# Performance work log

Hardware: AMD Instinct MI355X
Metric: run time of the kernel (lower is better)

The kernel has to match this reference:

```python
import jax, jax.numpy as jnp
import numpy as np

N_NODES = 30000
N_EDGES = 480000
N_GRAPHS = 64
IN_DIM = 128
HID = 64
NEG_SLOPE = 0.2  # PyG GATConv default leaky_relu slope


def setup_inputs() -> dict:
    key = jax.random.key(0)
    ks = jax.random.split(key, 16)
    x = jax.random.normal(ks[0], (N_NODES, IN_DIM), dtype=jnp.float32)
    src = jax.random.randint(ks[1], (N_EDGES,), 0, N_NODES, dtype=jnp.int32)
    dst = jax.random.randint(ks[2], (N_EDGES,), 0, N_NODES, dtype=jnp.int32)
    edge_index = jnp.stack([src, dst], axis=0)
    # evenly-sized sorted graph assignment so every graph id is populated
    batch = (jnp.arange(N_NODES, dtype=jnp.int32) * N_GRAPHS) // N_NODES
    sc1 = 1.0 / np.sqrt(IN_DIM)
    sc2 = 1.0 / np.sqrt(4 * HID)
    sc3 = 1.0 / np.sqrt(HID)
    return dict(
        x=x, edge_index=edge_index, batch=batch,
        W1=jax.random.normal(ks[3], (IN_DIM, 4 * HID), jnp.float32) * sc1,
        att_src1=jax.random.normal(ks[4], (4, HID), jnp.float32) * sc3,
        att_dst1=jax.random.normal(ks[5], (4, HID), jnp.float32) * sc3,
        b1=jnp.zeros((4 * HID,), jnp.float32),
        W2=jax.random.normal(ks[6], (4 * HID, HID), jnp.float32) * sc2,
        att_src2=jax.random.normal(ks[7], (1, HID), jnp.float32) * sc3,
        att_dst2=jax.random.normal(ks[8], (1, HID), jnp.float32) * sc3,
        b2=jnp.zeros((HID,), jnp.float32),
        w_fc1=jax.random.normal(ks[9], (HID, HID), jnp.float32) * sc3,
        b_fc1=jnp.zeros((HID,), jnp.float32),
        w_fc2=jax.random.normal(ks[10], (HID, 2), jnp.float32) * sc3,
        b_fc2=jnp.zeros((2,), jnp.float32),
    )


def _leaky_relu(v):
    return jnp.where(v > 0, v, NEG_SLOPE * v)


def _gat_conv(x, src, dst, W, att_src, att_dst, bias, heads, ch):
    n = x.shape[0]
    h = (x @ W).reshape(n, heads, ch)                      # [N,H,C]
    a_src = jnp.sum(h * att_src[None], axis=-1)            # [N,H]
    a_dst = jnp.sum(h * att_dst[None], axis=-1)            # [N,H]
    e = _leaky_relu(a_src[src] + a_dst[dst])               # [E,H]
    e_max = jax.ops.segment_max(e, dst, num_segments=n)
    e = jnp.exp(e - e_max[dst])
    denom = jax.ops.segment_sum(e, dst, num_segments=n)
    alpha = e / denom[dst]                                 # [E,H]
    msg = h[src] * alpha[:, :, None]                       # [E,H,C]
    out = jax.ops.segment_sum(msg, dst, num_segments=n)    # [N,H,C]
    return out.reshape(n, heads * ch) + bias


def reference(x, edge_index, batch, W1, att_src1, att_dst1, b1,
              W2, att_src2, att_dst2, b2, w_fc1, b_fc1, w_fc2, b_fc2):
    n = x.shape[0]
    # add self-loops (PyG GATConv default)
    loops = jnp.arange(n, dtype=edge_index.dtype)
    src = jnp.concatenate([edge_index[0], loops])
    dst = jnp.concatenate([edge_index[1], loops])
    h = jax.nn.relu(_gat_conv(x, src, dst, W1, att_src1, att_dst1, b1, 4, HID))
    h = jax.nn.relu(_gat_conv(h, src, dst, W2, att_src2, att_dst2, b2, 1, HID))
    g = jax.ops.segment_max(h, batch, num_segments=N_GRAPHS)  # global_max_pool [G,HID]
    g = jax.nn.relu(g @ w_fc1 + b_fc1)
    logits = g @ w_fc2 + b_fc2
    return jax.nn.log_softmax(logits, axis=1)
```

## Files before the change

kernel.cpp:

```cpp
#include <hip/hip_runtime.h>
#include <hip/hip_bf16.h>
#include <math.h>

#define N_NODES  30000
#define N_EDGESR 480000
#define E_TOT    (N_EDGESR + N_NODES)
#define N_GRAPHS 64
#define IN_DIM   128
#define HID      64
#define NEG_SLOPE 0.2f

typedef __attribute__((ext_vector_type(8))) short bf16x8;
typedef __attribute__((ext_vector_type(8))) unsigned short u16x8;
typedef __attribute__((ext_vector_type(4))) float f32x4;

__device__ __forceinline__ float lrelu(float v) { return v > 0.f ? v : NEG_SLOPE * v; }
__device__ __forceinline__ float bf2f(unsigned short u) { return __uint_as_float((unsigned)u << 16); }
__device__ __forceinline__ unsigned short f2bf(float f) {
    return __bfloat16_as_ushort(__float2bfloat16(f));
}

__global__ __launch_bounds__(256) void prep_kernel(const float* __restrict__ x,
                                                   const float* __restrict__ W1,
                                                   const float* __restrict__ W2,
                                                   unsigned short* __restrict__ xb,
                                                   unsigned short* __restrict__ w1t,
                                                   unsigned short* __restrict__ w2t,
                                                   int* __restrict__ counts,
                                                   unsigned* __restrict__ g) {
    int t = blockIdx.x * 256 + threadIdx.x;
    if (t < 480000) {
        int i = t * 8;
        float4 v0 = *reinterpret_cast<const float4*>(x + i);
        float4 v1 = *reinterpret_cast<const float4*>(x + i + 4);
        u16x8 o;
        o[0] = f2bf(v0.x); o[1] = f2bf(v0.y); o[2] = f2bf(v0.z); o[3] = f2bf(v0.w);
        o[4] = f2bf(v1.x); o[5] = f2bf(v1.y); o[6] = f2bf(v1.z); o[7] = f2bf(v1.w);
        *reinterpret_cast<u16x8*>(xb + i) = o;
    } else if (t < 510000) {
        counts[t - 480000] = 0;
    } else if (t < 514096) {
        g[t - 510000] = 0u;
    } else if (t < 546864) {
        int id = t - 514096;
        int k = id >> 8, n = id & 255;
        w1t[n * 128 + k] = f2bf(W1[id]);
    } else if (t < 563248) {
        int id = t - 546864;
        int k = id >> 6, n = id & 63;
        w2t[n * 256 + k] = f2bf(W2[id]);
    }
}

__global__ void edge_hist(const int* __restrict__ ei, int* __restrict__ counts) {
    int e = blockIdx.x * blockDim.x + threadIdx.x;
    if (e >= E_TOT) return;
    int d = (e < N_EDGESR) ? ei[N_EDGESR + e] : (e - N_EDGESR);
    atomicAdd(&counts[d], 1);
}

__global__ __launch_bounds__(1024) void scan_counts(const int* __restrict__ counts,
                                                    int* __restrict__ rowstart,
                                                    int* __restrict__ cursor) {
    __shared__ int bufA[1024];
    __shared__ int bufB[1024];
    const int t = threadIdx.x;
    const int CH = 30;
    int local[CH];
    int base = t * CH;
    int s = 0;
    #pragma unroll
    for (int i = 0; i < CH; ++i) {
        int idx = base + i;
        int c = (idx < N_NODES) ? counts[idx] : 0;
        local[i] = c; s += c;
    }
    bufA[t] = s;
    __syncthreads();
    int* a = bufA; int* b = bufB;
    for (int off = 1; off < 1024; off <<= 1) {
        int v = a[t] + ((t >= off) ? a[t - off] : 0);
        b[t] = v;
        __syncthreads();
        int* tmp = a; a = b; b = tmp;
    }
    int run = (t == 0) ? 0 : a[t - 1];
    #pragma unroll
    for (int i = 0; i < CH; ++i) {
        int idx = base + i;
        if (idx < N_NODES) { rowstart[idx] = run; cursor[idx] = run; run += local[i]; }
    }
    if (t == 0) rowstart[N_NODES] = E_TOT;
}

__global__ void edge_scatter(const int* __restrict__ ei, int* __restrict__ cursor,
                             int* __restrict__ srcidx) {
    int e = blockIdx.x * blockDim.x + threadIdx.x;
    if (e >= E_TOT) return;
    int s, d;
    if (e < N_EDGESR) { s = ei[e]; d = ei[N_EDGESR + e]; }
    else              { s = d = e - N_EDGESR; }
    int pos = atomicAdd(&cursor[d], 1);
    srcidx[pos] = s;
}

__global__ __launch_bounds__(256) void mfma_gemm1(const unsigned short* __restrict__ xb,
                                                  const unsigned short* __restrict__ w1t,
                                                  unsigned short* __restrict__ h1,
                                                  const float* __restrict__ att_src,
                                                  const float* __restrict__ att_dst,
                                                  float* __restrict__ a_src,
                                                  float* __restrict__ a_dst) {
    __shared__ __align__(16) unsigned short As[64 * 128];
    const int tid = threadIdx.x;
    const int w = tid >> 6;
    const int l = tid & 63;
    const int rowbase = blockIdx.x * 64;
    char* Ab = (char*)As;

    #pragma unroll
    for (int i = 0; i < 4; ++i) {
        int flat = i * 256 + tid;
        int r = flat >> 4;
        int cb = (flat & 15) * 16;
        int gr = rowbase + r; if (gr >= N_NODES) gr = N_NODES - 1;
        int4 v = *reinterpret_cast<const int4*>(xb + (size_t)gr * 128 + (cb >> 1));
        *reinterpret_cast<int4*>(Ab + r * 256 + (cb ^ ((r & 7) << 4))) = v;
    }
    __syncthreads();

    const int lm = l & 15, lh = l >> 4;
    f32x4 acc[4][4];
    #pragma unroll
    for (int rt = 0; rt < 4; ++rt)
        #pragma unroll
        for (int ct = 0; ct < 4; ++ct)
            acc[rt][ct] = (f32x4){0.f, 0.f, 0.f, 0.f};

    #pragma unroll
    for (int s = 0; s < 4; ++s) {
        bf16x8 bfr[4], afr[4];
        #pragma unroll
        for (int ct = 0; ct < 4; ++ct) {
            int n = w * 64 + ct * 16 + lm;
            bfr[ct] = *reinterpret_cast<const bf16x8*>(w1t + n * 128 + s * 32 + lh * 8);
        }
        #pragma unroll
        for (int rt = 0; rt < 4; ++rt) {
            int row = rt * 16 + lm;
            int cb = s * 64 + lh * 16;
            afr[rt] = *reinterpret_cast<const bf16x8*>(Ab + row * 256 + (cb ^ ((row & 7) << 4)));
        }
        #pragma unroll
        for (int rt = 0; rt < 4; ++rt)
            #pragma unroll
            for (int ct = 0; ct < 4; ++ct)
                acc[rt][ct] = __builtin_amdgcn_mfma_f32_16x16x32_bf16(bfr[ct], afr[rt], acc[rt][ct], 0, 0, 0);
    }

    #pragma unroll
    for (int rt = 0; rt < 4; ++rt) {
        int row = rowbase + rt * 16 + lm;
        float ps = 0.f, pd = 0.f;
        #pragma unroll
        for (int ct = 0; ct < 4; ++ct) {
            int col = w * 64 + ct * 16 + lh * 4;
            if (row < N_NODES) {
                ushort4 o;
                o.x = f2bf(acc[rt][ct][0]); o.y = f2bf(acc[rt][ct][1]);
                o.z = f2bf(acc[rt][ct][2]); o.w = f2bf(acc[rt][ct][3]);
                *reinterpret_cast<ushort4*>(h1 + (size_t)row * 256 + col) = o;
            }
            #pragma unroll
            for (int q = 0; q < 4; ++q) {
                ps += acc[rt][ct][q] * att_src[col + q];
                pd += acc[rt][ct][q] * att_dst[col + q];
            }
        }
        ps += __shfl_xor(ps, 16); ps += __shfl_xor(ps, 32);
        pd += __shfl_xor(pd, 16); pd += __shfl_xor(pd, 32);
        if (lh == 0 && row < N_NODES) {
            a_src[row * 4 + w] = ps;
            a_dst[row * 4 + w] = pd;
        }
    }
}

__global__ __launch_bounds__(256) void gat_agg1(const unsigned short* __restrict__ h1,
                                                const float* __restrict__ a_src,
                                                const float* __restrict__ a_dst,
                                                const int* __restrict__ rowstart,
                                                const int* __restrict__ srcidx,
                                                const float* __restrict__ b1,
                                                unsigned short* __restrict__ out1) {
    int n = (blockIdx.x * 256 + threadIdx.x) >> 6;
    int lane = threadIdx.x & 63;
    if (n >= N_NODES) return;
    int beg = rowstart[n], end = rowstart[n + 1];
    const int h    = lane & 3;
    const int slot = lane >> 2;
    const int half = lane >> 5;
    const int cl   = lane & 31;
    const int myhead = cl >> 3;
    float ad_h = a_dst[n * 4 + h];

    float acc[8] = {};
    float den_part = 0.f;
    int cb = beg;
    for (; cb + 16 <= end; cb += 16) {
        int s = srcidx[cb + slot];
        float w = __expf(lrelu(a_src[s * 4 + h] + ad_h));
        den_part += w;
        #pragma unroll
        for (int j = 0; j < 16; j += 2) {
            int e = j + half;
            float wj = __shfl(w, e * 4 + myhead);
            int   sj = __shfl(s, e * 4);
            u16x8 hv = *reinterpret_cast<const u16x8*>(h1 + (size_t)sj * 256 + cl * 8);
            #pragma unroll
            for (int q = 0; q < 8; ++q) acc[q] += wj * bf2f((unsigned short)hv[q]);
        }
    }
    if (cb < end) {
        int cnt = end - cb;
        float w = 0.f; int s = 0;
        if (slot < cnt) {
            s = srcidx[cb + slot];
            w = __expf(lrelu(a_src[s * 4 + h] + ad_h));
            den_part += w;
        }
        for (int j = 0; j < cnt; j += 2) {
            int e = j + half;
            float wj = __shfl(w, e * 4 + myhead);
            int   sj = __shfl(s, e * 4);
            if (e < cnt) {
                u16x8 hv = *reinterpret_cast<const u16x8*>(h1 + (size_t)sj * 256 + cl * 8);
                #pragma unroll
                for (int q = 0; q < 8; ++q) acc[q] += wj * bf2f((unsigned short)hv[q]);
            }
        }
    }
    #pragma unroll
    for (int q = 0; q < 8; ++q) acc[q] += __shfl_xor(acc[q], 32);
    #pragma unroll
    for (int off = 4; off < 64; off <<= 1) den_part += __shfl_xor(den_part, off);
    float inv = 1.f / __shfl(den_part, myhead);
    if (half == 0) {
        float4 bv0 = *reinterpret_cast<const float4*>(b1 + cl * 8);
        float4 bv1 = *reinterpret_cast<const float4*>(b1 + cl * 8 + 4);
        u16x8 o;
        o[0] = f2bf(fmaxf(acc[0] * inv + bv0.x, 0.f));
        o[1] = f2bf(fmaxf(acc[1] * inv + bv0.y, 0.f));
        o[2] = f2bf(fmaxf(acc[2] * inv + bv0.z, 0.f));
        o[3] = f2bf(fmaxf(acc[3] * inv + bv0.w, 0.f));
        o[4] = f2bf(fmaxf(acc[4] * inv + bv1.x, 0.f));
        o[5] = f2bf(fmaxf(acc[5] * inv + bv1.y, 0.f));
        o[6] = f2bf(fmaxf(acc[6] * inv + bv1.z, 0.f));
        o[7] = f2bf(fmaxf(acc[7] * inv + bv1.w, 0.f));
        __builtin_nontemporal_store(o, reinterpret_cast<u16x8*>(out1 + (size_t)n * 256 + cl * 8));
    }
}

__global__ __launch_bounds__(256) void mfma_gemm2(const unsigned short* __restrict__ a1b,
                                                  const unsigned short* __restrict__ w2t,
                                                  unsigned short* __restrict__ h2,
                                                  const float* __restrict__ att_src,
                                                  const float* __restrict__ att_dst,
                                                  float* __restrict__ a_src,
                                                  float* __restrict__ a_dst) {
    __shared__ __align__(16) unsigned short As[64 * 256];
    __shared__ float ps_s[4][64], pd_s[4][64];
    const int tid = threadIdx.x;
    const int w = tid >> 6, l = tid & 63;
    const int rowbase = blockIdx.x * 64;
    char* Ab = (char*)As;

    #pragma unroll
    for (int i = 0; i < 8; ++i) {
        int flat = i * 256 + tid;
        int r = flat >> 5;
        int cb = (flat & 31) * 16;
        int gr = rowbase + r; if (gr >= N_NODES) gr = N_NODES - 1;
        int4 v = *reinterpret_cast<const int4*>(a1b + (size_t)gr * 256 + (cb >> 1));
        *reinterpret_cast<int4*>(Ab + r * 512 + (cb ^ ((r & 7) << 4))) = v;
    }
    __syncthreads();

    const int lm = l & 15, lh = l >> 4;
    f32x4 acc[4];
    #pragma unroll
    for (int rt = 0; rt < 4; ++rt) acc[rt] = (f32x4){0.f, 0.f, 0.f, 0.f};

    #pragma unroll
    for (int s = 0; s < 8; ++s) {
        int n = w * 16 + lm;
        bf16x8 bf = *reinterpret_cast<const bf16x8*>(w2t + n * 256 + s * 32 + lh * 8);
        #pragma unroll
        for (int rt = 0; rt < 4; ++rt) {
            int row = rt * 16 + lm;
            int cb = s * 64 + lh * 16;
            bf16x8 af = *reinterpret_cast<const bf16x8*>(Ab + row * 512 + (cb ^ ((row & 7) << 4)));
            acc[rt] = __builtin_amdgcn_mfma_f32_16x16x32_bf16(bf, af, acc[rt], 0, 0, 0);
        }
    }

    #pragma unroll
    for (int rt = 0; rt < 4; ++rt) {
        int row = rowbase + rt * 16 + lm;
        int col = w * 16 + lh * 4;
        float ps = 0.f, pd = 0.f;
        if (row < N_NODES) {
            ushort4 o;
            o.x = f2bf(acc[rt][0]); o.y = f2bf(acc[rt][1]);
            o.z = f2bf(acc[rt][2]); o.w = f2bf(acc[rt][3]);
            *reinterpret_cast<ushort4*>(h2 + (size_t)row * 64 + col) = o;
        }
        #pragma unroll
        for (int q = 0; q < 4; ++q) {
            ps += acc[rt][q] * att_src[col + q];
            pd += acc[rt][q] * att_dst[col + q];
        }
        ps += __shfl_xor(ps, 16); ps += __shfl_xor(ps, 32);
        pd += __shfl_xor(pd, 16); pd += __shfl_xor(pd, 32);
        if (lh == 0) { ps_s[w][rt * 16 + lm] = ps; pd_s[w][rt * 16 + lm] = pd; }
    }
    __syncthreads();
    if (tid < 64) {
        int row = rowbase + tid;
        if (row < N_NODES) {
            a_src[row] = ps_s[0][tid] + ps_s[1][tid] + ps_s[2][tid] + ps_s[3][tid];
            a_dst[row] = pd_s[0][tid] + pd_s[1][tid] + pd_s[2][tid] + pd_s[3][tid];
        }
    }
}

__global__ __launch_bounds__(256) void gat_agg2_pool(const unsigned short* __restrict__ h2,
                                                     const float* __restrict__ a_src,
                                                     const float* __restrict__ a_dst,
                                                     const int* __restrict__ rowstart,
                                                     const int* __restrict__ srcidx,
                                                     const float* __restrict__ b2,
                                                     const int* __restrict__ batch,
                                                     unsigned* __restrict__ g) {
    __shared__ float sm[4][64];
    const int wid = threadIdx.x >> 6;
    const int lane = threadIdx.x & 63;
    const int n = blockIdx.x * 4 + wid;
    const int grp = lane >> 4;
    const int cl  = lane & 15;
    int beg = rowstart[n], end = rowstart[n + 1];
    float ad = a_dst[n];

    float4 acc = make_float4(0.f, 0.f, 0.f, 0.f);
    float den_part = 0.f;
    int cb = beg;
    for (; cb + 16 <= end; cb += 16) {
        float w = 0.f; int s = 0;
        if (lane < 16) {
            s = srcidx[cb + lane];
            w = __expf(lrelu(a_src[s] + ad));
            den_part += w;
        }
        #pragma unroll
        for (int j = 0; j < 16; j += 4) {
            float wj = __shfl(w, j + grp);
            int   sj = __shfl(s, j + grp);
            ushort4 hv = *reinterpret_cast<const ushort4*>(&h2[(size_t)sj * 64 + cl * 4]);
            acc.x += wj * bf2f(hv.x); acc.y += wj * bf2f(hv.y);
            acc.z += wj * bf2f(hv.z); acc.w += wj * bf2f(hv.w);
        }
    }
    if (cb < end) {
        int cnt = end - cb;
        float w = 0.f; int s = 0;
        if (lane < cnt) {
            s = srcidx[cb + lane];
            w = __expf(lrelu(a_src[s] + ad));
            den_part += w;
        }
        for (int j = 0; j < cnt; j += 4) {
            float wj = __shfl(w, j + grp);
            int   sj = __shfl(s, j + grp);
            if (j + grp < cnt) {
                ushort4 hv = *reinterpret_cast<const ushort4*>(&h2[(size_t)sj * 64 + cl * 4]);
                acc.x += wj * bf2f(hv.x); acc.y += wj * bf2f(hv.y);
                acc.z += wj * bf2f(hv.z); acc.w += wj * bf2f(hv.w);
            }
        }
    }
    #pragma unroll
    for (int off = 16; off < 64; off <<= 1) {
        acc.x += __shfl_xor(acc.x, off);
        acc.y += __shfl_xor(acc.y, off);
        acc.z += __shfl_xor(acc.z, off);
        acc.w += __shfl_xor(acc.w, off);
    }
    #pragma unroll
    for (int off = 1; off < 64; off <<= 1) den_part += __shfl_xor(den_part, off);
    float inv = 1.f / den_part;
    float4 bv = *reinterpret_cast<const float4*>(&b2[cl * 4]);
    if (lane < 16) {
        float4 val;
        val.x = fmaxf(acc.x * inv + bv.x, 0.f);
        val.y = fmaxf(acc.y * inv + bv.y, 0.f);
        val.z = fmaxf(acc.z * inv + bv.z, 0.f);
        val.w = fmaxf(acc.w * inv + bv.w, 0.f);
        *reinterpret_cast<float4*>(&sm[wid][cl * 4]) = val;
    }
    __syncthreads();
    int b0 = batch[blockIdx.x * 4];
    int b3 = batch[blockIdx.x * 4 + 3];
    if (b0 == b3) {
        if (threadIdx.x < 64) {
            float v = fmaxf(fmaxf(sm[0][threadIdx.x], sm[1][threadIdx.x]),
                            fmaxf(sm[2][threadIdx.x], sm[3][threadIdx.x]));
            atomicMax(&g[b0 * 64 + threadIdx.x], __float_as_uint(v));
        }
    } else {
        if (lane < 16) {
            int bb = batch[n];
            #pragma unroll
            for (int k = 0; k < 4; ++k)
                atomicMax(&g[bb * 64 + cl * 4 + k], __float_as_uint(sm[wid][cl * 4 + k]));
        }
    }
}

__global__ __launch_bounds__(256) void head_kernel(const float* __restrict__ g,
                                                   const float* __restrict__ w_fc1,
                                                   const float* __restrict__ b_fc1,
                                                   const float* __restrict__ w_fc2,
                                                   const float* __restrict__ b_fc2,
                                                   float* __restrict__ out) {
    __shared__ float gs[64][65];
    __shared__ float hs[64][65];
    int t = threadIdx.x;
    #pragma unroll
    for (int it = 0; it < 16; ++it) {
        int flat = it * 256 + t;
        gs[flat >> 6][flat & 63] = g[flat];
    }
    __syncthreads();
    #pragma unroll
    for (int it = 0; it < 16; ++it) {
        int flat = it * 256 + t;
        int i = flat >> 6, j = flat & 63;
        float s = b_fc1[j];
        #pragma unroll 8
        for (int k = 0; k < 64; ++k) s += gs[i][k] * w_fc1[k * 64 + j];
        hs[i][j] = fmaxf(s, 0.f);
    }
    __syncthreads();
    if (t < 64) {
        float l0 = b_fc2[0], l1 = b_fc2[1];
        #pragma unroll 8
        for (int k = 0; k < 64; ++k) {
            float v = hs[t][k];
            l0 += v * w_fc2[k * 2];
            l1 += v * w_fc2[k * 2 + 1];
        }
        float mx = fmaxf(l0, l1);
        float lse = mx + logf(__expf(l0 - mx) + __expf(l1 - mx));
        out[t * 2]     = l0 - lse;
        out[t * 2 + 1] = l1 - lse;
    }
}

extern "C" void kernel_launch(void* const* d_in, const int* in_sizes, int n_in,
                              void* d_out, int out_size, void* d_ws, size_t ws_size,
                              hipStream_t stream) {
    const float* x        = (const float*)d_in[0];
    const int*   ei       = (const int*)d_in[1];
    const int*   batch    = (const int*)d_in[2];
    const float* W1       = (const float*)d_in[3];
    const float* att_src1 = (const float*)d_in[4];
    const float* att_dst1 = (const float*)d_in[5];
    const float* b1       = (const float*)d_in[6];
    const float* W2       = (const float*)d_in[7];
    const float* att_src2 = (const float*)d_in[8];
    const float* att_dst2 = (const float*)d_in[9];
    const float* b2       = (const float*)d_in[10];
    const float* w_fc1    = (const float*)d_in[11];
    const float* b_fc1    = (const float*)d_in[12];
    const float* w_fc2    = (const float*)d_in[13];
    const float* b_fc2    = (const float*)d_in[14];

    char* ws = (char*)d_ws;
    size_t off = 0;
    auto alloc = [&](size_t bytes) -> char* {
        char* p = ws + off;
        off += (bytes + 255) & ~(size_t)255;
        return p;
    };
    unsigned short* xb   = (unsigned short*)alloc((size_t)N_NODES * 128 * 2);
    unsigned short* w1t  = (unsigned short*)alloc((size_t)256 * 128 * 2);
    unsigned short* w2t  = (unsigned short*)alloc((size_t)64 * 256 * 2);
    unsigned short* h1   = (unsigned short*)alloc((size_t)N_NODES * 256 * 2);
    unsigned short* out1 = (unsigned short*)alloc((size_t)N_NODES * 256 * 2);
    unsigned short* h2   = (unsigned short*)alloc((size_t)N_NODES * 64 * 2);
    float*    as1        = (float*)alloc((size_t)N_NODES * 4 * 4);
    float*    ad1        = (float*)alloc((size_t)N_NODES * 4 * 4);
    float*    as2        = (float*)alloc((size_t)N_NODES * 4);
    float*    ad2        = (float*)alloc((size_t)N_NODES * 4);
    int*      counts     = (int*)alloc((size_t)N_NODES * 4);
    int*      rowstart   = (int*)alloc((size_t)(N_NODES + 4) * 4);
    int*      cursor     = (int*)alloc((size_t)(N_NODES + 4) * 4);
    int*      srcidx     = (int*)alloc((size_t)E_TOT * 4);
    unsigned* g          = (unsigned*)alloc((size_t)N_GRAPHS * HID * 4);

    prep_kernel<<<2201, 256, 0, stream>>>(x, W1, W2, xb, w1t, w2t, counts, g);
    edge_hist<<<(E_TOT + 255) / 256, 256, 0, stream>>>(ei, counts);
    scan_counts<<<1, 1024, 0, stream>>>(counts, rowstart, cursor);
    edge_scatter<<<(E_TOT + 255) / 256, 256, 0, stream>>>(ei, cursor, srcidx);
    mfma_gemm1<<<(N_NODES + 63) / 64, 256, 0, stream>>>(xb, w1t, h1, att_src1, att_dst1, as1, ad1);
    gat_agg1<<<7500, 256, 0, stream>>>(h1, as1, ad1, rowstart, srcidx, b1, out1);
    mfma_gemm2<<<(N_NODES + 63) / 64, 256, 0, stream>>>(out1, w2t, h2, att_src2, att_dst2, as2, ad2);
    gat_agg2_pool<<<7500, 256, 0, stream>>>(h2, as2, ad2, rowstart, srcidx, b2, batch, g);
    head_kernel<<<1, 256, 0, stream>>>((const float*)g, w_fc1, b_fc1, w_fc2, b_fc2, (float*)d_out);
}
```

Measured before the change: 191.1 us.

## Fuse edge histogram into prep and edge scatter into GEMM1 launch

The edge-histogram pass is merged into the prep kernel, with counts zeroed by a memset issued beforehand. The independent edge-scatter and first MFMA GEMM now share one launch, split by block index, so they can run concurrently. gat_agg1 drops to 128-thread blocks with two nodes per block. The goal is fewer kernel launches and better overlap of small, latency-bound stages, at the cost of a heterogeneous block mix and an extra memset call.

New measurement: 199.4 us. 4.3% more time.

```diff
diff --git a/kernel.cpp b/kernel.cpp
--- a/kernel.cpp
+++ b/kernel.cpp
@@ -20,14 +20,15 @@
     return __bfloat16_as_ushort(__float2bfloat16(f));
 }
 
-__global__ __launch_bounds__(256) void prep_kernel(const float* __restrict__ x,
-                                                   const float* __restrict__ W1,
-                                                   const float* __restrict__ W2,
-                                                   unsigned short* __restrict__ xb,
-                                                   unsigned short* __restrict__ w1t,
-                                                   unsigned short* __restrict__ w2t,
-                                                   int* __restrict__ counts,
-                                                   unsigned* __restrict__ g) {
+__global__ __launch_bounds__(256) void prep_hist_kernel(const float* __restrict__ x,
+                                                        const float* __restrict__ W1,
+                                                        const float* __restrict__ W2,
+                                                        const int* __restrict__ ei,
+                                                        unsigned short* __restrict__ xb,
+                                                        unsigned short* __restrict__ w1t,
+                                                        unsigned short* __restrict__ w2t,
+                                                        int* __restrict__ counts,
+                                                        unsigned* __restrict__ g) {
     int t = blockIdx.x * 256 + threadIdx.x;
     if (t < 480000) {
         int i = t * 8;
@@ -37,26 +38,21 @@
         o[0] = f2bf(v0.x); o[1] = f2bf(v0.y); o[2] = f2bf(v0.z); o[3] = f2bf(v0.w);
         o[4] = f2bf(v1.x); o[5] = f2bf(v1.y); o[6] = f2bf(v1.z); o[7] = f2bf(v1.w);
         *reinterpret_cast<u16x8*>(xb + i) = o;
-    } else if (t < 510000) {
-        counts[t - 480000] = 0;
-    } else if (t < 514096) {
-        g[t - 510000] = 0u;
-    } else if (t < 546864) {
-        int id = t - 514096;
+    } else if (t < 484096) {
+        g[t - 480000] = 0u;
+    } else if (t < 516864) {
+        int id = t - 484096;
         int k = id >> 8, n = id & 255;
         w1t[n * 128 + k] = f2bf(W1[id]);
-    } else if (t < 563248) {
-        int id = t - 546864;
+    } else if (t < 533248) {
+        int id = t - 516864;
         int k = id >> 6, n = id & 63;
         w2t[n * 256 + k] = f2bf(W2[id]);
-    }
-}
-
-__global__ void edge_hist(const int* __restrict__ ei, int* __restrict__ counts) {
-    int e = blockIdx.x * blockDim.x + threadIdx.x;
-    if (e >= E_TOT) return;
-    int d = (e < N_EDGESR) ? ei[N_EDGESR + e] : (e - N_EDGESR);
-    atomicAdd(&counts[d], 1);
+    } else if (t < 533248 + E_TOT) {
+        int e = t - 533248;
+        int d = (e < N_EDGESR) ? ei[N_EDGESR + e] : (e - N_EDGESR);
+        atomicAdd(&counts[d], 1);
+    }
 }
 
 __global__ __launch_bounds__(1024) void scan_counts(const int* __restrict__ counts,
@@ -93,29 +89,33 @@
     if (t == 0) rowstart[N_NODES] = E_TOT;
 }
 
-__global__ void edge_scatter(const int* __restrict__ ei, int* __restrict__ cursor,
-                             int* __restrict__ srcidx) {
-    int e = blockIdx.x * blockDim.x + threadIdx.x;
-    if (e >= E_TOT) return;
-    int s, d;
-    if (e < N_EDGESR) { s = ei[e]; d = ei[N_EDGESR + e]; }
-    else              { s = d = e - N_EDGESR; }
-    int pos = atomicAdd(&cursor[d], 1);
-    srcidx[pos] = s;
-}
-
-__global__ __launch_bounds__(256) void mfma_gemm1(const unsigned short* __restrict__ xb,
-                                                  const unsigned short* __restrict__ w1t,
-                                                  unsigned short* __restrict__ h1,
-                                                  const float* __restrict__ att_src,
-                                                  const float* __restrict__ att_dst,
-                                                  float* __restrict__ a_src,
-                                                  float* __restrict__ a_dst) {
+#define SCAT_B 1993
+__global__ __launch_bounds__(256) void scatter_gemm1(const int* __restrict__ ei,
+                                                     int* __restrict__ cursor,
+                                                     int* __restrict__ srcidx,
+                                                     const unsigned short* __restrict__ xb,
+                                                     const unsigned short* __restrict__ w1t,
+                                                     unsigned short* __restrict__ h1,
+                                                     const float* __restrict__ att_src,
+                                                     const float* __restrict__ att_dst,
+                                                     float* __restrict__ a_src,
+                                                     float* __restrict__ a_dst) {
     __shared__ __align__(16) unsigned short As[64 * 128];
+    const int b = blockIdx.x;
     const int tid = threadIdx.x;
+    if (b < SCAT_B) {
+        int e = b * 256 + tid;
+        if (e >= E_TOT) return;
+        int s, d;
+        if (e < N_EDGESR) { s = ei[e]; d = ei[N_EDGESR + e]; }
+        else              { s = d = e - N_EDGESR; }
+        int pos = atomicAdd(&cursor[d], 1);
+        srcidx[pos] = s;
+        return;
+    }
     const int w = tid >> 6;
     const int l = tid & 63;
-    const int rowbase = blockIdx.x * 64;
+    const int rowbase = (b - SCAT_B) * 64;
     char* Ab = (char*)As;
 
     #pragma unroll
@@ -186,14 +186,14 @@
     }
 }
 
-__global__ __launch_bounds__(256) void gat_agg1(const unsigned short* __restrict__ h1,
+__global__ __launch_bounds__(128) void gat_agg1(const unsigned short* __restrict__ h1,
                                                 const float* __restrict__ a_src,
                                                 const float* __restrict__ a_dst,
                                                 const int* __restrict__ rowstart,
                                                 const int* __restrict__ srcidx,
                                                 const float* __restrict__ b1,
                                                 unsigned short* __restrict__ out1) {
-    int n = (blockIdx.x * 256 + threadIdx.x) >> 6;
+    int n = blockIdx.x * 2 + (threadIdx.x >> 6);
     int lane = threadIdx.x & 63;
     if (n >= N_NODES) return;
     int beg = rowstart[n], end = rowstart[n + 1];
@@ -508,12 +508,12 @@
     int*      srcidx     = (int*)alloc((size_t)E_TOT * 4);
     unsigned* g          = (unsigned*)alloc((size_t)N_GRAPHS * HID * 4);
 
-    prep_kernel<<<2201, 256, 0, stream>>>(x, W1, W2, xb, w1t, w2t, counts, g);
-    edge_hist<<<(E_TOT + 255) / 256, 256, 0, stream>>>(ei, counts);
+    hipMemsetAsync(counts, 0, (size_t)N_NODES * 4, stream);
+    prep_hist_kernel<<<4076, 256, 0, stream>>>(x, W1, W2, ei, xb, w1t, w2t, counts, g);
     scan_counts<<<1, 1024, 0, stream>>>(counts, rowstart, cursor);
-    edge_scatter<<<(E_TOT + 255) / 256, 256, 0, stream>>>(ei, cursor, srcidx);
-    mfma_gemm1<<<(N_NODES + 63) / 64, 256, 0, stream>>>(xb, w1t, h1, att_src1, att_dst1, as1, ad1);
-    gat_agg1<<<7500, 256, 0, stream>>>(h1, as1, ad1, rowstart, srcidx, b1, out1);
+    scatter_gemm1<<<SCAT_B + 469, 256, 0, stream>>>(ei, cursor, srcidx,
+                                                    xb, w1t, h1, att_src1, att_dst1, as1, ad1);
+    gat_agg1<<<15000, 128, 0, stream>>>(h1, as1, ad1, rowstart, srcidx, b1, out1);
     mfma_gemm2<<<(N_NODES + 63) / 64, 256, 0, stream>>>(out1, w2t, h2, att_src2, att_dst2, as2, ad2);
     gat_agg2_pool<<<7500, 256, 0, stream>>>(h2, as2, ad2, rowstart, srcidx, b2, batch, g);
     head_kernel<<<1, 256, 0, stream>>>((const float*)g, w_fc1, b_fc1, w_fc2, b_fc2, (float*)d_out);
```
